# Performance work log

Measured on AMD Instinct MI355X. Metric: run time of the kernel, lower is better.

The kernel has to match this reference:

```python
import jax, jax.numpy as jnp
import numpy as np

DIM = 1024
NH = 16
HD = DIM // NH  # 64
WINDOW = 8      # window_size; flash window=(WINDOW-1, -1) with causal=True
EPS_NORM = 1e-6


def _rmsnorm(h, w):
    # RMSNorm over last dim (full model dim, applied before head split)
    return h * jax.lax.rsqrt(jnp.mean(h * h, axis=-1, keepdims=True) + EPS_NORM) * w


def _rope(h, cos, sin):
    # h: [bv, L, NH, HD]; cos/sin: [L, HD//2]; torch view-as-complex pairs adjacent elems
    hr = h[..., 0::2]
    hi = h[..., 1::2]
    c = cos[None, :, None, :]
    s = sin[None, :, None, :]
    out_r = hr * c - hi * s
    out_i = hr * s + hi * c
    return jnp.stack([out_r, out_i], axis=-1).reshape(h.shape)


def setup_inputs() -> dict:
    key = jax.random.key(0)
    ks = jax.random.split(key, 8)
    bv, f, nlt = 1, 16, 1472
    b = bv * f
    L = f * nlt
    wscale = DIM ** -0.5
    x = jax.random.normal(ks[0], (b, nlt, DIM), jnp.float32)
    # standard RoPE tables, base 10000, d//2 frequencies
    pos = jnp.arange(L, dtype=jnp.float32)[:, None]
    inv_freq = 1.0 / (10000.0 ** (jnp.arange(HD // 2, dtype=jnp.float32) / (HD // 2)))
    ang = pos * inv_freq[None, :]
    inp = {
        'x': x,
        'freqs_cos': jnp.cos(ang),
        'freqs_sin': jnp.sin(ang),
        'q_w': jax.random.normal(ks[1], (DIM, DIM), jnp.float32) * wscale,
        'q_b': jnp.zeros((DIM,), jnp.float32),
        'k_w': jax.random.normal(ks[2], (DIM, DIM), jnp.float32) * wscale,
        'k_b': jnp.zeros((DIM,), jnp.float32),
        'v_w': jax.random.normal(ks[3], (DIM, DIM), jnp.float32) * wscale,
        'v_b': jnp.zeros((DIM,), jnp.float32),
        'o_w': jax.random.normal(ks[4], (DIM, DIM), jnp.float32) * wscale,
        'o_b': jnp.zeros((DIM,), jnp.float32),
        'norm_q_w': jnp.ones((DIM,), jnp.float32),
        'norm_k_w': jnp.ones((DIM,), jnp.float32),
        'bv': 1,
        'f': 16,
        'nlt': 1472,
    }
    return inp


def reference(x, freqs_cos, freqs_sin, q_w, q_b, k_w, k_b, v_w, v_b, o_w, o_b,
              norm_q_w, norm_k_w, bv, f, nlt):
    b, s = x.shape[:2]  # b = bv*f, s = nlt
    q = _rmsnorm(x @ q_w.T + q_b, norm_q_w)
    k = _rmsnorm(x @ k_w.T + k_b, norm_k_w)
    v = (x @ v_w.T + v_b).reshape(bv, f, s, NH, HD)
    # RoPE over flattened (frame, token) positions
    q4 = q.reshape(bv, f * s, NH, HD)
    k4 = k.reshape(bv, f * s, NH, HD)
    qr = _rope(q4, freqs_cos, freqs_sin)
    kr = _rope(k4, freqs_cos, freqs_sin)
    # temporal layout: [bv*nlt, f, NH, HD] (attend over frames per latent token)
    qr = qr.reshape(bv, f, s, NH, HD).transpose(0, 2, 1, 3, 4).reshape(bv * s, f, NH, HD)
    kr = kr.reshape(bv, f, s, NH, HD).transpose(0, 2, 1, 3, 4).reshape(bv * s, f, NH, HD)
    vr = v.transpose(0, 2, 1, 3, 4).reshape(bv * s, f, NH, HD)
    # causal sliding-window mask over frames: j <= i and i - j < WINDOW
    fi = jnp.arange(f)
    mask = (fi[None, :] <= fi[:, None]) & (fi[:, None] - fi[None, :] < WINDOW)  # [f, f]
    scores = jnp.einsum('bqhd,bkhd->bhqk', qr, kr) / np.float32(np.sqrt(HD))
    scores = jnp.where(mask[None, None], scores, jnp.float32(-1e30))
    attn = jax.nn.softmax(scores, axis=-1)
    o = jnp.einsum('bhqk,bkhd->bqhd', attn, vr)  # [bv*nlt, f, NH, HD]
    o = o.reshape(bv, s, f, NH, HD).transpose(0, 2, 1, 3, 4).reshape(bv * f, s, DIM)
    return o @ o_w.T + o_b
```

## Files before the change

kernel.cpp:

```cpp
#include <hip/hip_runtime.h>
#include <hip/hip_bf16.h>
#include <math.h>

typedef __bf16 bf16;
typedef bf16 bf16x8 __attribute__((ext_vector_type(8)));
typedef bf16 bf16x4 __attribute__((ext_vector_type(4)));
typedef float f32x4 __attribute__((ext_vector_type(4)));

#define NFRM 16
#define SEQ  1472
#define TOK  (NFRM * SEQ)
#define DIM_ 1024
#define NH_  16
#define HD_  64

__device__ __forceinline__ void load_lds_16B(const void* g, void* l) {
  __builtin_amdgcn_global_load_lds(
      (const __attribute__((address_space(1))) unsigned int*)g,
      (__attribute__((address_space(3))) unsigned int*)l,
      16, 0, 0);
}

__global__ __launch_bounds__(256) void cvt_bf16(const float* __restrict__ s,
                                                bf16* __restrict__ d, int n) {
  size_t i = ((size_t)blockIdx.x * 256 + threadIdx.x) * 8;
  if (i >= (size_t)n) return;
  f32x4 a = *(const f32x4*)(s + i);
  f32x4 b = *(const f32x4*)(s + i + 4);
  bf16x8 o;
  o[0] = (bf16)a[0]; o[1] = (bf16)a[1]; o[2] = (bf16)a[2]; o[3] = (bf16)a[3];
  o[4] = (bf16)b[0]; o[5] = (bf16)b[1]; o[6] = (bf16)b[2]; o[7] = (bf16)b[3];
  *(bf16x8*)(d + i) = o;
}

template <typename OutT>
__device__ __forceinline__ void gemm_body(const bf16* __restrict__ A,
                                          const bf16* __restrict__ B,
                                          const float* __restrict__ bias,
                                          OutT* __restrict__ C,
                                          bf16* As, bf16* Bs) {
  const int tid  = threadIdx.x;
  const int wave = tid >> 6;
  const int lane = tid & 63;
  const size_t am0 = (size_t)blockIdx.x * 128;
  const size_t bn0 = (size_t)blockIdx.y * 128;

  f32x4 acc[4][4];
#pragma unroll
  for (int i = 0; i < 4; ++i)
#pragma unroll
    for (int j = 0; j < 4; ++j) {
      f32x4 z = {0.f, 0.f, 0.f, 0.f};
      acc[i][j] = z;
    }

  const int wm   = (wave >> 1) * 64;
  const int wn   = (wave & 1) * 64;
  const int frow = lane & 15;
  const int fko  = (lane >> 4) * 8;

  for (int k0 = 0; k0 < DIM_; k0 += 32) {
#pragma unroll
    for (int it = 0; it < 2; ++it) {
      const int cb  = it * 256 + wave * 64;
      const int c   = cb + lane;
      const int row = c >> 2;
      const int kc  = (c & 3) * 8;
      load_lds_16B(A + (am0 + row) * DIM_ + k0 + kc, As + cb * 8);
      load_lds_16B(B + (bn0 + row) * DIM_ + k0 + kc, Bs + cb * 8);
    }
    __syncthreads();
    bf16x8 af[4], bfv[4];
#pragma unroll
    for (int i = 0; i < 4; ++i)
      af[i] = *(const bf16x8*)(As + (wm + i * 16 + frow) * 32 + fko);
#pragma unroll
    for (int j = 0; j < 4; ++j)
      bfv[j] = *(const bf16x8*)(Bs + (wn + j * 16 + frow) * 32 + fko);
#pragma unroll
    for (int i = 0; i < 4; ++i)
#pragma unroll
      for (int j = 0; j < 4; ++j)
        acc[i][j] = __builtin_amdgcn_mfma_f32_16x16x32_bf16(af[i], bfv[j],
                                                            acc[i][j], 0, 0, 0);
    __syncthreads();
  }

  const int cl = lane & 15;
  const int rq = (lane >> 4) * 4;
#pragma unroll
  for (int i = 0; i < 4; ++i)
#pragma unroll
    for (int j = 0; j < 4; ++j) {
      const int nc   = (int)bn0 + wn + j * 16 + cl;
      const float bb = bias[nc];
#pragma unroll
      for (int r = 0; r < 4; ++r) {
        const size_t mr = am0 + wm + i * 16 + rq + r;
        C[mr * DIM_ + nc] = (OutT)(acc[i][j][r] + bb);
      }
    }
}

__global__ __launch_bounds__(256) void gemm_qkv(
    const bf16* __restrict__ A,
    const bf16* __restrict__ Bq, const bf16* __restrict__ Bk,
    const bf16* __restrict__ Bv,
    const float* __restrict__ bq, const float* __restrict__ bk,
    const float* __restrict__ bv,
    bf16* __restrict__ Cq, bf16* __restrict__ Ck, bf16* __restrict__ Cv) {
  __shared__ __align__(16) bf16 As[128 * 32];
  __shared__ __align__(16) bf16 Bs[128 * 32];
  const int z = blockIdx.z;
  const bf16* B    = (z == 0) ? Bq : (z == 1) ? Bk : Bv;
  const float* bia = (z == 0) ? bq : (z == 1) ? bk : bv;
  bf16* C          = (z == 0) ? Cq : (z == 1) ? Ck : Cv;
  gemm_body<bf16>(A, B, bia, C, As, Bs);
}

__global__ __launch_bounds__(256) void gemm_out(
    const bf16* __restrict__ A, const bf16* __restrict__ B,
    const float* __restrict__ bias, float* __restrict__ C) {
  __shared__ __align__(16) bf16 As[128 * 32];
  __shared__ __align__(16) bf16 Bs[128 * 32];
  gemm_body<float>(A, B, bias, C, As, Bs);
}

__global__ __launch_bounds__(256) void norm_rope(
    bf16* __restrict__ q, bf16* __restrict__ k,
    const float* __restrict__ nqw, const float* __restrict__ nkw,
    const float* __restrict__ fcos, const float* __restrict__ fsin) {
  const int t   = blockIdx.x;
  const int fi  = blockIdx.y;
  const int tid = threadIdx.x;
  const int lane = tid & 63, wave = tid >> 6;
  const size_t row  = (size_t)fi * SEQ + t;
  const size_t base = row * DIM_;
  __shared__ float red[4];

  const int e0 = tid * 4;
  const int j0 = (e0 & 63) >> 1;
  const float c0 = fcos[row * 32 + j0],     s0 = fsin[row * 32 + j0];
  const float c1 = fcos[row * 32 + j0 + 1], s1 = fsin[row * 32 + j0 + 1];

  for (int which = 0; which < 2; ++which) {
    bf16* buf      = which ? k : q;
    const float* w = which ? nkw : nqw;
    bf16x4 xv = *(const bf16x4*)(buf + base + e0);
    float x0 = (float)xv[0], x1 = (float)xv[1];
    float x2 = (float)xv[2], x3 = (float)xv[3];
    float ss = x0 * x0 + x1 * x1 + x2 * x2 + x3 * x3;
#pragma unroll
    for (int off = 32; off > 0; off >>= 1) ss += __shfl_down(ss, off);
    if (lane == 0) red[wave] = ss;
    __syncthreads();
    const float tot = red[0] + red[1] + red[2] + red[3];
    const float rs  = rsqrtf(tot * (1.0f / 1024.0f) + 1e-6f);
    x0 *= rs * w[e0];     x1 *= rs * w[e0 + 1];
    x2 *= rs * w[e0 + 2]; x3 *= rs * w[e0 + 3];
    bf16x4 ov;
    ov[0] = (bf16)(x0 * c0 - x1 * s0);
    ov[1] = (bf16)(x0 * s0 + x1 * c0);
    ov[2] = (bf16)(x2 * c1 - x3 * s1);
    ov[3] = (bf16)(x2 * s1 + x3 * c1);
    *(bf16x4*)(buf + base + e0) = ov;
    __syncthreads();
  }
}

__global__ __launch_bounds__(256) void attn_win(
    const bf16* __restrict__ q, const bf16* __restrict__ k,
    const bf16* __restrict__ v, bf16* __restrict__ o) {
  const int t   = blockIdx.x;
  const int h   = blockIdx.y;
  const int tid = threadIdx.x;
  __shared__ float qs[16 * 65], ks[16 * 65], vs[16 * 65];
  __shared__ float ps[16 * 16];

  {
    const int r  = tid >> 4;
    const int c4 = (tid & 15) * 4;
    const size_t g = ((size_t)r * SEQ + t) * DIM_ + h * HD_ + c4;
    bf16x4 qv = *(const bf16x4*)(q + g);
    bf16x4 kv = *(const bf16x4*)(k + g);
    bf16x4 vv = *(const bf16x4*)(v + g);
    const int l = r * 65 + c4;
#pragma unroll
    for (int i = 0; i < 4; ++i) {
      qs[l + i] = (float)qv[i];
      ks[l + i] = (float)kv[i];
      vs[l + i] = (float)vv[i];
    }
  }
  __syncthreads();

  const int fq = tid >> 4, fk = tid & 15;
  float s = 0.f;
#pragma unroll
  for (int d = 0; d < 64; ++d) s += qs[fq * 65 + d] * ks[fk * 65 + d];
  const bool valid = (fk <= fq) && (fq - fk < 8);
  s = valid ? s * 0.125f : -1e30f;

  float m = s;
#pragma unroll
  for (int off = 8; off > 0; off >>= 1) m = fmaxf(m, __shfl_xor(m, off, 16));
  const float p = __expf(s - m);
  float sum = p;
#pragma unroll
  for (int off = 8; off > 0; off >>= 1) sum += __shfl_xor(sum, off, 16);
  ps[fq * 16 + fk] = p / sum;
  __syncthreads();

  const int d  = tid & 63;
  const int r0 = tid >> 6;
#pragma unroll
  for (int rep = 0; rep < 4; ++rep) {
    const int row = r0 * 4 + rep;
    float acc = 0.f;
#pragma unroll
    for (int f2 = 0; f2 < 16; ++f2) acc += ps[row * 16 + f2] * vs[f2 * 65 + d];
    o[((size_t)row * SEQ + t) * DIM_ + h * HD_ + d] = (bf16)acc;
  }
}

extern "C" void kernel_launch(void* const* d_in, const int* in_sizes, int n_in,
                              void* d_out, int out_size, void* d_ws,
                              size_t ws_size, hipStream_t stream) {
  const float* x    = (const float*)d_in[0];
  const float* fcos = (const float*)d_in[1];
  const float* fsin = (const float*)d_in[2];
  const float* q_w  = (const float*)d_in[3];
  const float* q_b  = (const float*)d_in[4];
  const float* k_w  = (const float*)d_in[5];
  const float* k_b  = (const float*)d_in[6];
  const float* v_w  = (const float*)d_in[7];
  const float* v_b  = (const float*)d_in[8];
  const float* o_w  = (const float*)d_in[9];
  const float* o_b  = (const float*)d_in[10];
  const float* nqw  = (const float*)d_in[11];
  const float* nkw  = (const float*)d_in[12];
  float* out = (float*)d_out;

  char* ws = (char*)d_ws;
  const size_t SZ  = (size_t)TOK * DIM_ * 2;
  const size_t WSZ = (size_t)DIM_ * DIM_ * 2;
  bf16* xb = (bf16*)(ws);
  bf16* wq = (bf16*)(ws + SZ);
  bf16* wk = (bf16*)(ws + SZ + WSZ);
  bf16* wv = (bf16*)(ws + SZ + 2 * WSZ);
  bf16* wo = (bf16*)(ws + SZ + 3 * WSZ);
  bf16* qq = (bf16*)(ws + SZ + 4 * WSZ);
  bf16* kk = (bf16*)(ws + SZ + 4 * WSZ + SZ);
  bf16* vv = (bf16*)(ws + SZ + 4 * WSZ + 2 * SZ);
  bf16* om = xb;

  const int NTOT = TOK * DIM_;
  const int NW   = DIM_ * DIM_;

  cvt_bf16<<<NTOT / 2048, 256, 0, stream>>>(x, xb, NTOT);
  cvt_bf16<<<NW / 2048, 256, 0, stream>>>(q_w, wq, NW);
  cvt_bf16<<<NW / 2048, 256, 0, stream>>>(k_w, wk, NW);
  cvt_bf16<<<NW / 2048, 256, 0, stream>>>(v_w, wv, NW);
  cvt_bf16<<<NW / 2048, 256, 0, stream>>>(o_w, wo, NW);

  dim3 gq(TOK / 128, DIM_ / 128, 3);
  gemm_qkv<<<gq, 256, 0, stream>>>(xb, wq, wk, wv, q_b, k_b, v_b, qq, kk, vv);

  norm_rope<<<dim3(SEQ, NFRM), 256, 0, stream>>>(qq, kk, nqw, nkw, fcos, fsin);

  attn_win<<<dim3(SEQ, NH_), 256, 0, stream>>>(qq, kk, vv, om);

  gemm_out<<<dim3(TOK / 128, DIM_ / 128), 256, 0, stream>>>(om, wo, o_b, out);
}
```

Before: 576.4 us.

## Batch weight casts, use wave-per-row norm/rope, and MFMA windowed attention

The four weight casts are merged into one launch. norm_rope now gives each row to a single wave that handles q and k together with 16-element vector loads and shuffle-only reductions, so the shared-memory barriers go away. attn_win now runs one block per token across all heads. It stages K and V into LDS with global_load_lds, computes scores with bf16 MFMA, and stores the probabilities as bf16. This cuts launch count, redundant loads and fp32 LDS traffic, at the cost of bf16 rounding of the probabilities and heavy LDS use per block.

```diff
diff --git a/kernel.cpp b/kernel.cpp
--- a/kernel.cpp
+++ b/kernel.cpp
@@ -13,6 +13,7 @@
 #define DIM_ 1024
 #define NH_  16
 #define HD_  64
+#define KROW 1032
 
 __device__ __forceinline__ void load_lds_16B(const void* g, void* l) {
   __builtin_amdgcn_global_load_lds(
@@ -25,6 +26,23 @@
                                                 bf16* __restrict__ d, int n) {
   size_t i = ((size_t)blockIdx.x * 256 + threadIdx.x) * 8;
   if (i >= (size_t)n) return;
+  f32x4 a = *(const f32x4*)(s + i);
+  f32x4 b = *(const f32x4*)(s + i + 4);
+  bf16x8 o;
+  o[0] = (bf16)a[0]; o[1] = (bf16)a[1]; o[2] = (bf16)a[2]; o[3] = (bf16)a[3];
+  o[4] = (bf16)b[0]; o[5] = (bf16)b[1]; o[6] = (bf16)b[2]; o[7] = (bf16)b[3];
+  *(bf16x8*)(d + i) = o;
+}
+
+__global__ __launch_bounds__(256) void cvt_w4(
+    const float* __restrict__ w0, const float* __restrict__ w1,
+    const float* __restrict__ w2, const float* __restrict__ w3,
+    bf16* __restrict__ d0, bf16* __restrict__ d1,
+    bf16* __restrict__ d2, bf16* __restrict__ d3) {
+  const int z = blockIdx.y;
+  const float* s = (z == 0) ? w0 : (z == 1) ? w1 : (z == 2) ? w2 : w3;
+  bf16* d       = (z == 0) ? d0 : (z == 1) ? d1 : (z == 2) ? d2 : d3;
+  size_t i = ((size_t)blockIdx.x * 256 + threadIdx.x) * 8;
   f32x4 a = *(const f32x4*)(s + i);
   f32x4 b = *(const f32x4*)(s + i + 4);
   bf16x8 o;
@@ -130,96 +148,150 @@
     bf16* __restrict__ q, bf16* __restrict__ k,
     const float* __restrict__ nqw, const float* __restrict__ nkw,
     const float* __restrict__ fcos, const float* __restrict__ fsin) {
-  const int t   = blockIdx.x;
-  const int fi  = blockIdx.y;
-  const int tid = threadIdx.x;
-  const int lane = tid & 63, wave = tid >> 6;
-  const size_t row  = (size_t)fi * SEQ + t;
+  const int lane = threadIdx.x & 63, wave = threadIdx.x >> 6;
+  const size_t row  = (size_t)blockIdx.x * 4 + wave;
   const size_t base = row * DIM_;
-  __shared__ float red[4];
-
-  const int e0 = tid * 4;
-  const int j0 = (e0 & 63) >> 1;
-  const float c0 = fcos[row * 32 + j0],     s0 = fsin[row * 32 + j0];
-  const float c1 = fcos[row * 32 + j0 + 1], s1 = fsin[row * 32 + j0 + 1];
-
-  for (int which = 0; which < 2; ++which) {
-    bf16* buf      = which ? k : q;
-    const float* w = which ? nkw : nqw;
-    bf16x4 xv = *(const bf16x4*)(buf + base + e0);
-    float x0 = (float)xv[0], x1 = (float)xv[1];
-    float x2 = (float)xv[2], x3 = (float)xv[3];
-    float ss = x0 * x0 + x1 * x1 + x2 * x2 + x3 * x3;
-#pragma unroll
-    for (int off = 32; off > 0; off >>= 1) ss += __shfl_down(ss, off);
-    if (lane == 0) red[wave] = ss;
-    __syncthreads();
-    const float tot = red[0] + red[1] + red[2] + red[3];
-    const float rs  = rsqrtf(tot * (1.0f / 1024.0f) + 1e-6f);
-    x0 *= rs * w[e0];     x1 *= rs * w[e0 + 1];
-    x2 *= rs * w[e0 + 2]; x3 *= rs * w[e0 + 3];
-    bf16x4 ov;
-    ov[0] = (bf16)(x0 * c0 - x1 * s0);
-    ov[1] = (bf16)(x0 * s0 + x1 * c0);
-    ov[2] = (bf16)(x2 * c1 - x3 * s1);
-    ov[3] = (bf16)(x2 * s1 + x3 * c1);
-    *(bf16x4*)(buf + base + e0) = ov;
-    __syncthreads();
-  }
-}
-
-__global__ __launch_bounds__(256) void attn_win(
+  const int e0 = lane * 16;
+  const int j0 = (lane & 3) * 8;
+
+  float cs[8], sn[8];
+#pragma unroll
+  for (int i = 0; i < 8; ++i) {
+    cs[i] = fcos[row * 32 + j0 + i];
+    sn[i] = fsin[row * 32 + j0 + i];
+  }
+
+  bf16x8 qa = *(const bf16x8*)(q + base + e0);
+  bf16x8 qb = *(const bf16x8*)(q + base + e0 + 8);
+  bf16x8 ka = *(const bf16x8*)(k + base + e0);
+  bf16x8 kb = *(const bf16x8*)(k + base + e0 + 8);
+
+  float xq[16], xk[16];
+#pragma unroll
+  for (int i = 0; i < 8; ++i) {
+    xq[i] = (float)qa[i]; xq[8 + i] = (float)qb[i];
+    xk[i] = (float)ka[i]; xk[8 + i] = (float)kb[i];
+  }
+  float sq = 0.f, sk = 0.f;
+#pragma unroll
+  for (int i = 0; i < 16; ++i) { sq += xq[i] * xq[i]; sk += xk[i] * xk[i]; }
+#pragma unroll
+  for (int off = 32; off > 0; off >>= 1) {
+    sq += __shfl_xor(sq, off);
+    sk += __shfl_xor(sk, off);
+  }
+  const float rq = rsqrtf(sq * (1.0f / 1024.0f) + 1e-6f);
+  const float rk = rsqrtf(sk * (1.0f / 1024.0f) + 1e-6f);
+#pragma unroll
+  for (int i = 0; i < 16; ++i) {
+    xq[i] *= rq * nqw[e0 + i];
+    xk[i] *= rk * nkw[e0 + i];
+  }
+  bf16x8 oa, ob, oc, od;
+#pragma unroll
+  for (int p = 0; p < 8; ++p) {
+    const float c = cs[p], s = sn[p];
+    const float q0 = xq[2 * p], q1 = xq[2 * p + 1];
+    const float k0 = xk[2 * p], k1 = xk[2 * p + 1];
+    const float qr = q0 * c - q1 * s, qi = q0 * s + q1 * c;
+    const float kr = k0 * c - k1 * s, ki = k0 * s + k1 * c;
+    if (p < 4) { oa[2 * p] = (bf16)qr; oa[2 * p + 1] = (bf16)qi;
+                 oc[2 * p] = (bf16)kr; oc[2 * p + 1] = (bf16)ki; }
+    else       { ob[2 * p - 8] = (bf16)qr; ob[2 * p - 7] = (bf16)qi;
+                 od[2 * p - 8] = (bf16)kr; od[2 * p - 7] = (bf16)ki; }
+  }
+  *(bf16x8*)(q + base + e0)     = oa;
+  *(bf16x8*)(q + base + e0 + 8) = ob;
+  *(bf16x8*)(k + base + e0)     = oc;
+  *(bf16x8*)(k + base + e0 + 8) = od;
+}
+
+__global__ __launch_bounds__(512, 4) void attn_win(
     const bf16* __restrict__ q, const bf16* __restrict__ k,
     const bf16* __restrict__ v, bf16* __restrict__ o) {
-  const int t   = blockIdx.x;
-  const int h   = blockIdx.y;
-  const int tid = threadIdx.x;
-  __shared__ float qs[16 * 65], ks[16 * 65], vs[16 * 65];
-  __shared__ float ps[16 * 16];
-
-  {
-    const int r  = tid >> 4;
-    const int c4 = (tid & 15) * 4;
-    const size_t g = ((size_t)r * SEQ + t) * DIM_ + h * HD_ + c4;
-    bf16x4 qv = *(const bf16x4*)(q + g);
-    bf16x4 kv = *(const bf16x4*)(k + g);
-    bf16x4 vv = *(const bf16x4*)(v + g);
-    const int l = r * 65 + c4;
+  __shared__ __align__(16) bf16 ks[16 * KROW];
+  __shared__ __align__(16) bf16 vs[16 * KROW];
+  __shared__ __align__(16) bf16 ps[16 * 256];
+  const int t    = blockIdx.x;
+  const int tid  = threadIdx.x;
+  const int wave = tid >> 6, lane = tid & 63;
+
+#pragma unroll
+  for (int i = 0; i < 4; ++i) {
+    const int j = wave * 4 + i;
+    const int r = j >> 1, half = j & 1;
+    const size_t g = ((size_t)r * SEQ + t) * DIM_ + half * 512 + lane * 8;
+    load_lds_16B(k + g, ks + r * KROW + half * 512);
+    load_lds_16B(v + g, vs + r * KROW + half * 512);
+  }
+  __syncthreads();
+
+  const int fl  = lane & 15;
+  const int kq  = (lane >> 4) * 8;
+#pragma unroll
+  for (int hh = 0; hh < 2; ++hh) {
+    const int h = wave * 2 + hh;
+    const size_t qg = ((size_t)fl * SEQ + t) * DIM_ + h * HD_ + kq;
+    bf16x8 aq0 = *(const bf16x8*)(q + qg);
+    bf16x8 aq1 = *(const bf16x8*)(q + qg + 32);
+    const int ko = fl * KROW + h * HD_ + kq;
+    bf16x8 bk0 = *(const bf16x8*)(ks + ko);
+    bf16x8 bk1 = *(const bf16x8*)(ks + ko + 32);
+    f32x4 sc = {0.f, 0.f, 0.f, 0.f};
+    sc = __builtin_amdgcn_mfma_f32_16x16x32_bf16(aq0, bk0, sc, 0, 0, 0);
+    sc = __builtin_amdgcn_mfma_f32_16x16x32_bf16(aq1, bk1, sc, 0, 0, 0);
+#pragma unroll
+    for (int r = 0; r < 4; ++r) {
+      const int row = (lane >> 4) * 4 + r;
+      const bool valid = (fl <= row) && (row - fl < 8);
+      float s = valid ? sc[r] * 0.125f : -1e30f;
+      float m = s;
+#pragma unroll
+      for (int off = 8; off > 0; off >>= 1) m = fmaxf(m, __shfl_xor(m, off));
+      const float e = __expf(s - m);
+      float su = e;
+#pragma unroll
+      for (int off = 8; off > 0; off >>= 1) su += __shfl_xor(su, off);
+      ps[h * 256 + row * 16 + fl] = (bf16)(e / su);
+    }
+  }
+  __syncthreads();
+
+  const int h3 = tid >> 5;
+  const int dc = (tid >> 2) & 7;
+  const int fg = tid & 3;
+  bf16x8 pr[8];
+#pragma unroll
+  for (int i = 0; i < 4; ++i) {
+    pr[2 * i]     = *(const bf16x8*)(ps + h3 * 256 + (fg * 4 + i) * 16);
+    pr[2 * i + 1] = *(const bf16x8*)(ps + h3 * 256 + (fg * 4 + i) * 16 + 8);
+  }
+  float acc[4][8];
+#pragma unroll
+  for (int i = 0; i < 4; ++i)
+#pragma unroll
+    for (int d = 0; d < 8; ++d) acc[i][d] = 0.f;
+
+  const bf16* vb = vs + h3 * HD_ + dc * 8;
+#pragma unroll
+  for (int fk2 = 0; fk2 < 16; ++fk2) {
+    bf16x8 vv8 = *(const bf16x8*)(vb + fk2 * KROW);
+    float vf[8];
+#pragma unroll
+    for (int d = 0; d < 8; ++d) vf[d] = (float)vv8[d];
 #pragma unroll
     for (int i = 0; i < 4; ++i) {
-      qs[l + i] = (float)qv[i];
-      ks[l + i] = (float)kv[i];
-      vs[l + i] = (float)vv[i];
-    }
-  }
-  __syncthreads();
-
-  const int fq = tid >> 4, fk = tid & 15;
-  float s = 0.f;
-#pragma unroll
-  for (int d = 0; d < 64; ++d) s += qs[fq * 65 + d] * ks[fk * 65 + d];
-  const bool valid = (fk <= fq) && (fq - fk < 8);
-  s = valid ? s * 0.125f : -1e30f;
-
-  float m = s;
-#pragma unroll
-  for (int off = 8; off > 0; off >>= 1) m = fmaxf(m, __shfl_xor(m, off, 16));
-  const float p = __expf(s - m);
-  float sum = p;
-#pragma unroll
-  for (int off = 8; off > 0; off >>= 1) sum += __shfl_xor(sum, off, 16);
-  ps[fq * 16 + fk] = p / sum;
-  __syncthreads();
-
-  const int d  = tid & 63;
-  const int r0 = tid >> 6;
-#pragma unroll
-  for (int rep = 0; rep < 4; ++rep) {
-    const int row = r0 * 4 + rep;
-    float acc = 0.f;
-#pragma unroll
-    for (int f2 = 0; f2 < 16; ++f2) acc += ps[row * 16 + f2] * vs[f2 * 65 + d];
-    o[((size_t)row * SEQ + t) * DIM_ + h * HD_ + d] = (bf16)acc;
+      const float pp = (float)((fk2 < 8) ? pr[2 * i][fk2] : pr[2 * i + 1][fk2 - 8]);
+#pragma unroll
+      for (int d = 0; d < 8; ++d) acc[i][d] += pp * vf[d];
+    }
+  }
+#pragma unroll
+  for (int i = 0; i < 4; ++i) {
+    bf16x8 ov;
+#pragma unroll
+    for (int d = 0; d < 8; ++d) ov[d] = (bf16)acc[i][d];
+    *(bf16x8*)(o + ((size_t)(fg * 4 + i) * SEQ + t) * DIM_ + h3 * HD_ + dc * 8) = ov;
   }
 }
 
@@ -258,17 +330,15 @@
   const int NW   = DIM_ * DIM_;
 
   cvt_bf16<<<NTOT / 2048, 256, 0, stream>>>(x, xb, NTOT);
-  cvt_bf16<<<NW / 2048, 256, 0, stream>>>(q_w, wq, NW);
-  cvt_bf16<<<NW / 2048, 256, 0, stream>>>(k_w, wk, NW);
-  cvt_bf16<<<NW / 2048, 256, 0, stream>>>(v_w, wv, NW);
-  cvt_bf16<<<NW / 2048, 256, 0, stream>>>(o_w, wo, NW);
+  cvt_w4<<<dim3(NW / 2048, 4), 256, 0, stream>>>(q_w, k_w, v_w, o_w,
+                                                 wq, wk, wv, wo);
 
   dim3 gq(TOK / 128, DIM_ / 128, 3);
   gemm_qkv<<<gq, 256, 0, stream>>>(xb, wq, wk, wv, q_b, k_b, v_b, qq, kk, vv);
 
-  norm_rope<<<dim3(SEQ, NFRM), 256, 0, stream>>>(qq, kk, nqw, nkw, fcos, fsin);
-
-  attn_win<<<dim3(SEQ, NH_), 256, 0, stream>>>(qq, kk, vv, om);
+  norm_rope<<<TOK / 4, 256, 0, stream>>>(qq, kk, nqw, nkw, fcos, fsin);
+
+  attn_win<<<SEQ, 512, 0, stream>>>(qq, kk, vv, om);
 
   gemm_out<<<dim3(TOK / 128, DIM_ / 128), 256, 0, stream>>>(om, wo, o_b, out);
 }
```

New measurement: 680.7 us. 1.18x slower.
